# Kernel optimization log

Hardware: AMD Instinct MI355X
Metric: run time of the kernel (lower is better)

## Reference

```python
import jax, jax.numpy as jnp
import numpy as np

DIM = 4096
HEAD_DIM = 512
ROPE_DIM = 64
NOPE_DIM = HEAD_DIM - ROPE_DIM  # 448
RATIO = 4
COFF = 2  # overlap since ratio == 4
EPS = 1e-6
NEG = -1e30
COMPRESS_ROPE_THETA = 40000.0


def _hadamard(n):
    H = np.array([[1.0]], dtype=np.float32)
    while H.shape[0] < n:
        H = np.block([[H, H], [H, -H]])
    return (H / np.sqrt(n)).astype(np.float32)

H_MAT = jnp.asarray(_hadamard(HEAD_DIM))  # [512, 512], orthonormal Hadamard


def setup_inputs() -> dict:
    key = jax.random.key(0)
    ks = jax.random.split(key, 5)
    b, s = 4, 4096
    x = jax.random.normal(ks[0], (b, s, DIM), dtype=jnp.float32)
    W_kv = jax.random.normal(ks[1], (COFF * HEAD_DIM, DIM), dtype=jnp.float32) * 0.02
    W_gate = jax.random.normal(ks[2], (COFF * HEAD_DIM, DIM), dtype=jnp.float32) * 0.02
    ape = jax.random.normal(ks[3], (RATIO, COFF * HEAD_DIM), dtype=jnp.float32) * 0.02
    norm_w = jnp.ones((HEAD_DIM,), dtype=jnp.float32)
    # rotary table over compressed-block positions
    nb = s // RATIO
    inv_freq = 1.0 / (COMPRESS_ROPE_THETA ** (jnp.arange(0, ROPE_DIM, 2, dtype=jnp.float32) / ROPE_DIM))
    ang = jnp.arange(nb, dtype=jnp.float32)[:, None] * inv_freq[None, :]  # [nb, 32]
    freqs_cis = jnp.stack([jnp.cos(ang), jnp.sin(ang)], axis=-1)  # [nb, 32, 2]
    return {"x": x, "W_kv": W_kv, "W_gate": W_gate, "ape": ape,
            "norm_w": norm_w, "freqs_cis": freqs_cis, "start_pos": 0}


def _overlap_transform(t, fill):
    # t: [b, nb, RATIO, 2*d] -> [b, nb, 2*RATIO, d]
    b, nb, r, dd = t.shape
    d = dd // 2
    prev_first = jnp.concatenate(
        [jnp.full((b, 1, r, d), fill, t.dtype), t[:, :-1, :, :d]], axis=1)
    return jnp.concatenate([prev_first, t[..., d:]], axis=2)


def reference(x, W_kv, W_gate, ape, norm_w, freqs_cis, start_pos):
    b, s, _ = x.shape
    nb = s // RATIO
    # block-wise projections with absolute-within-block positional bias
    kv = jnp.einsum('bsd,od->bso', x, W_kv).reshape(b, nb, RATIO, COFF * HEAD_DIM) + ape
    score = jnp.einsum('bsd,od->bso', x, W_gate).reshape(b, nb, RATIO, COFF * HEAD_DIM)
    # overlap with previous block: [b, nb, 2*RATIO, HEAD_DIM]
    kv_w = _overlap_transform(kv, 0.0)
    sc_w = _overlap_transform(score, NEG)
    # channelwise softmax-gated pooling over the 2*RATIO window
    w = jax.nn.softmax(sc_w, axis=2)
    pooled = jnp.sum(w * kv_w, axis=2)  # [b, nb, HEAD_DIM]
    # RMSNorm
    var = jnp.mean(jnp.square(pooled), axis=-1, keepdims=True)
    pooled = norm_w * (pooled * jax.lax.rsqrt(var + EPS))
    # rotary on the rope slice
    nope, rope = pooled[..., :NOPE_DIM], pooled[..., NOPE_DIM:]
    rp = rope.reshape(b, nb, ROPE_DIM // 2, 2)
    xr, xi = rp[..., 0], rp[..., 1]
    fr, fi = freqs_cis[None, :, :, 0], freqs_cis[None, :, :, 1]
    rot = jnp.stack([xr * fr - xi * fi, xr * fi + xi * fr], axis=-1).reshape(b, nb, ROPE_DIM)
    out = jnp.concatenate([nope, rot], axis=-1)  # [b, nb, HEAD_DIM]
    # Hadamard rotation (rotate_activation)
    out = out @ H_MAT
    return out
```

## Files before the change

### kernel.cpp

```cpp
#include <hip/hip_runtime.h>
#include <hip/hip_bf16.h>
#include <stdint.h>

#define M_ROWS 16384
#define N_COLS 2048
#define K_DIM  4096
#define NEGV   -1e30f

typedef __bf16 bfv8 __attribute__((ext_vector_type(8)));
typedef float  f32x4 __attribute__((ext_vector_type(4)));
typedef unsigned short u16;

static __device__ __forceinline__ u16 f32_to_bf16_rne(float f) {
  union { float f; unsigned int u; } v; v.f = f;
  unsigned int u = v.u;
  u += 0x7fffu + ((u >> 16) & 1u);
  return (u16)(u >> 16);
}

static __device__ __forceinline__ float b2f(u16 b) {
  union { unsigned int u; float f; } v; v.u = ((unsigned int)b) << 16;
  return v.f;
}

__global__ __launch_bounds__(256) void k_cvt_x(const float* __restrict__ in,
                                               u16* __restrict__ out, long n) {
  long i = (long)blockIdx.x * blockDim.x + threadIdx.x;
  long base = i * 8;
  if (base >= n) return;
  float4 a = *(const float4*)(in + base);
  float4 b = *(const float4*)(in + base + 4);
  union { u16 s[8]; uint4 v; } o;
  o.s[0] = f32_to_bf16_rne(a.x); o.s[1] = f32_to_bf16_rne(a.y);
  o.s[2] = f32_to_bf16_rne(a.z); o.s[3] = f32_to_bf16_rne(a.w);
  o.s[4] = f32_to_bf16_rne(b.x); o.s[5] = f32_to_bf16_rne(b.y);
  o.s[6] = f32_to_bf16_rne(b.z); o.s[7] = f32_to_bf16_rne(b.w);
  *(uint4*)(out + base) = o.v;
}

__global__ __launch_bounds__(256) void k_cvt_w(const float* __restrict__ wkv,
                                               const float* __restrict__ wg,
                                               u16* __restrict__ out) {
  long i = (long)blockIdx.x * blockDim.x + threadIdx.x;
  long base = i * 8;
  const float* src = (base < 4194304L) ? (wkv + base) : (wg + (base - 4194304L));
  float4 a = *(const float4*)(src);
  float4 b = *(const float4*)(src + 4);
  union { u16 s[8]; uint4 v; } o;
  o.s[0] = f32_to_bf16_rne(a.x); o.s[1] = f32_to_bf16_rne(a.y);
  o.s[2] = f32_to_bf16_rne(a.z); o.s[3] = f32_to_bf16_rne(a.w);
  o.s[4] = f32_to_bf16_rne(b.x); o.s[5] = f32_to_bf16_rne(b.y);
  o.s[6] = f32_to_bf16_rne(b.z); o.s[7] = f32_to_bf16_rne(b.w);
  *(uint4*)(out + base) = o.v;
}

#define GLD16(g, l) __builtin_amdgcn_global_load_lds( \
    (const __attribute__((address_space(1))) unsigned int*)(g), \
    (__attribute__((address_space(3))) unsigned int*)(l), 16, 0, 0)

#define SB0 __builtin_amdgcn_sched_barrier(0)
#define BAR __builtin_amdgcn_s_barrier()
#define VM4 asm volatile("s_waitcnt vmcnt(4)" ::: "memory")

__global__ __launch_bounds__(512, 2) void k_gemm(const u16* __restrict__ A,
                                                 const u16* __restrict__ B,
                                                 u16* __restrict__ C) {
  __shared__ u16 lds[65536];

  const int tid  = threadIdx.x;
  const int wid  = tid >> 6;
  const int lane = tid & 63;
  const int wr = wid >> 2, wc = wid & 3;
  const int fr = lane & 15, fq = lane >> 4;

  int o = blockIdx.x;
  int swz = (o & 7) * 64 + (o >> 3);
  const int bm = swz >> 3, bn = swz & 7;
  const int gm0 = bm << 8, gn0 = bn << 8;

  int aoff[8], boff[4];
#pragma unroll
  for (int mi = 0; mi < 8; ++mi) {
    int row = (wr << 7) + (mi << 4) + fr;
    int Gp = (((row & 1) << 2) | fq) ^ ((row >> 1) & 7);
    aoff[mi] = (row >> 1) * 64 + Gp * 8;
  }
#pragma unroll
  for (int ni = 0; ni < 4; ++ni) {
    int row = (wc << 6) + (ni << 4) + fr;
    int Gp = (((row & 1) << 2) | fq) ^ ((row >> 1) & 7);
    boff[ni] = (row >> 1) * 64 + Gp * 8;
  }

  const int s0 = tid, s1 = 512 + tid;
  const int l0 = s0 >> 3, G0 = (s0 & 7) ^ (l0 & 7);
  const int r0 = 2 * l0 + (G0 >> 2), g0 = (G0 & 3) << 3;
  const int l1 = s1 >> 3, G1 = (s1 & 7) ^ (l1 & 7);
  const int r1 = 2 * l1 + (G1 >> 2), g1 = (G1 & 3) << 3;
  const u16* pA0 = A + ((size_t)(gm0 + r0) << 12) + g0;
  const u16* pA1 = A + ((size_t)(gm0 + r1) << 12) + g1;
  const u16* pB0 = B + ((size_t)(gn0 + r0) << 12) + g0;
  const u16* pB1 = B + ((size_t)(gn0 + r1) << 12) + g1;
  const int du0 = wid << 9;
  const int du1 = 4096 + (wid << 9);

#define STAGE_A(Q, KK, KTN) do { \
  GLD16(pA0 + (KTN) + (KK) * 32, &lds[(Q) * 16384 + (KK) * 8192 + du0]); \
  GLD16(pA1 + (KTN) + (KK) * 32, &lds[(Q) * 16384 + (KK) * 8192 + du1]); } while (0)
#define STAGE_B(Q, KK, KTN) do { \
  GLD16(pB0 + (KTN) + (KK) * 32, &lds[32768 + (Q) * 16384 + (KK) * 8192 + du0]); \
  GLD16(pB1 + (KTN) + (KK) * 32, &lds[32768 + (Q) * 16384 + (KK) * 8192 + du1]); } while (0)
#define LDA(P, KK, MI) (*(const bfv8*)&lds[(P) * 16384 + (KK) * 8192 + aoff[MI]])
#define LDB(P, KK, NI) (*(const bfv8*)&lds[32768 + (P) * 16384 + (KK) * 8192 + boff[NI]])
#define MF(AV, BV, MI, NI) acc[MI][NI] = __builtin_amdgcn_mfma_f32_16x16x32_bf16(AV, BV, acc[MI][NI], 0, 0, 0)
#define MF4(AV, MI) do { MF(AV, b0, MI, 0); MF(AV, b1, MI, 1); MF(AV, b2, MI, 2); MF(AV, b3, MI, 3); } while (0)

  f32x4 acc[8][4];
#pragma unroll
  for (int i = 0; i < 8; ++i)
#pragma unroll
    for (int j = 0; j < 4; ++j) acc[i][j] = (f32x4){0.f, 0.f, 0.f, 0.f};

  STAGE_A(0, 0, 0); STAGE_B(0, 0, 0); STAGE_A(0, 1, 0); STAGE_B(0, 1, 0);
  SB0; VM4; BAR; SB0;

  bfv8 a0, a1, a2, a3, a4, a5, a6, a7, b0, b1, b2, b3;

#define KTILE(P, Q, KTN) do { \
  a0 = LDA(P, 0, 0); a1 = LDA(P, 0, 1); a2 = LDA(P, 0, 2); a3 = LDA(P, 0, 3); \
  b0 = LDB(P, 0, 0); b1 = LDB(P, 0, 1); b2 = LDB(P, 0, 2); b3 = LDB(P, 0, 3); \
  STAGE_A(Q, 0, KTN); \
  SB0; BAR; SB0; \
  __builtin_amdgcn_s_setprio(1); \
  MF4(a0, 0); MF4(a1, 1); MF4(a2, 2); MF4(a3, 3); \
  __builtin_amdgcn_s_setprio(0); SB0; \
  a4 = LDA(P, 0, 4); a5 = LDA(P, 0, 5); a6 = LDA(P, 0, 6); a7 = LDA(P, 0, 7); \
  STAGE_B(Q, 0, KTN); \
  SB0; VM4; BAR; SB0; \
  __builtin_amdgcn_s_setprio(1); \
  MF4(a4, 4); MF4(a5, 5); MF4(a6, 6); MF4(a7, 7); \
  __builtin_amdgcn_s_setprio(0); SB0; \
  a0 = LDA(P, 1, 0); a1 = LDA(P, 1, 1); a2 = LDA(P, 1, 2); a3 = LDA(P, 1, 3); \
  b0 = LDB(P, 1, 0); b1 = LDB(P, 1, 1); b2 = LDB(P, 1, 2); b3 = LDB(P, 1, 3); \
  STAGE_A(Q, 1, KTN); \
  SB0; BAR; SB0; \
  __builtin_amdgcn_s_setprio(1); \
  MF4(a0, 0); MF4(a1, 1); MF4(a2, 2); MF4(a3, 3); \
  __builtin_amdgcn_s_setprio(0); SB0; \
  a4 = LDA(P, 1, 4); a5 = LDA(P, 1, 5); a6 = LDA(P, 1, 6); a7 = LDA(P, 1, 7); \
  STAGE_B(Q, 1, KTN); \
  SB0; VM4; BAR; SB0; \
  __builtin_amdgcn_s_setprio(1); \
  MF4(a4, 4); MF4(a5, 5); MF4(a6, 6); MF4(a7, 7); \
  __builtin_amdgcn_s_setprio(0); SB0; \
} while (0)

  for (int i = 0; i < 32; ++i) {
    const int kt1 = (2 * i + 1) << 6;
    const int kt2 = (i == 31) ? 0 : (2 * i + 2) << 6;
    KTILE(0, 1, kt1);
    KTILE(1, 0, kt2);
  }

#pragma unroll
  for (int mi = 0; mi < 8; ++mi) {
    int row = gm0 + (wr << 7) + (mi << 4) + (fq << 2);
#pragma unroll
    for (int ni = 0; ni < 4; ++ni) {
      int col = gn0 + (wc << 6) + (ni << 4) + fr;
#pragma unroll
      for (int j = 0; j < 4; ++j)
        C[(size_t)(row + j) * N_COLS + col] = f32_to_bf16_rne(acc[mi][ni][j]);
    }
  }
#undef KTILE
#undef STAGE_A
#undef STAGE_B
#undef LDA
#undef LDB
#undef MF
#undef MF4
}

__global__ __launch_bounds__(256) void k_pool(const u16* __restrict__ kvsc,
                                              const float* __restrict__ ape,
                                              const float* __restrict__ norm_w,
                                              const float* __restrict__ freqs,
                                              float* __restrict__ out) {
  __shared__ float sm[512];
  __shared__ float red[8];
  const int tid = threadIdx.x;
  const int bid = blockIdx.x;
  const int b = bid >> 10, ib = bid & 1023;

  float ss = 0.f;
#pragma unroll
  for (int cc = 0; cc < 2; ++cc) {
    int c = tid + (cc << 8);
    float kvv[8], scv[8];
    if (ib > 0) {
      size_t mb = ((size_t)b * 4096 + (size_t)(ib - 1) * 4);
#pragma unroll
      for (int p = 0; p < 4; ++p) {
        size_t ro = (mb + p) * N_COLS;
        kvv[p] = b2f(kvsc[ro + c]) + ape[p * 1024 + c];
        scv[p] = b2f(kvsc[ro + 1024 + c]);
      }
    } else {
#pragma unroll
      for (int p = 0; p < 4; ++p) { kvv[p] = 0.f; scv[p] = NEGV; }
    }
    size_t mb2 = ((size_t)b * 4096 + (size_t)ib * 4);
#pragma unroll
    for (int r = 0; r < 4; ++r) {
      size_t ro = (mb2 + r) * N_COLS;
      kvv[4 + r] = b2f(kvsc[ro + 512 + c]) + ape[r * 1024 + 512 + c];
      scv[4 + r] = b2f(kvsc[ro + 1024 + 512 + c]);
    }
    float mx = scv[0];
#pragma unroll
    for (int p = 1; p < 8; ++p) mx = fmaxf(mx, scv[p]);
    float se = 0.f, ac = 0.f;
#pragma unroll
    for (int p = 0; p < 8; ++p) {
      float e = __expf(scv[p] - mx);
      se += e; ac += e * kvv[p];
    }
    float pooled = ac / se;
    sm[c] = pooled;
    ss += pooled * pooled;
  }
#pragma unroll
  for (int m = 1; m < 64; m <<= 1) ss += __shfl_xor(ss, m, 64);
  if ((tid & 63) == 0) red[tid >> 6] = ss;
  __syncthreads();
  float sumsq = red[0] + red[1] + red[2] + red[3];
  float scale = rsqrtf(sumsq * (1.f / 512.f) + 1e-6f);
  sm[tid]       = sm[tid]       * scale * norm_w[tid];
  sm[tid + 256] = sm[tid + 256] * scale * norm_w[tid + 256];
  __syncthreads();
  if (tid < 32) {
    int j = tid;
    float xr = sm[448 + 2 * j], xi = sm[449 + 2 * j];
    float fr = freqs[((size_t)ib * 32 + j) * 2];
    float fi = freqs[((size_t)ib * 32 + j) * 2 + 1];
    sm[448 + 2 * j] = xr * fr - xi * fi;
    sm[449 + 2 * j] = xr * fi + xi * fr;
  }
  __syncthreads();
#pragma unroll
  for (int k = 0; k < 9; ++k) {
    int low = tid & ((1 << k) - 1);
    int i0 = ((tid >> k) << (k + 1)) | low;
    int i1 = i0 | (1 << k);
    float a = sm[i0], bb = sm[i1];
    sm[i0] = a + bb; sm[i1] = a - bb;
    __syncthreads();
  }
  const float OSC = 0.044194173824159216f;
  size_t ob = (size_t)bid * 512;
  out[ob + tid]       = sm[tid] * OSC;
  out[ob + tid + 256] = sm[tid + 256] * OSC;
}

extern "C" void kernel_launch(void* const* d_in, const int* in_sizes, int n_in,
                              void* d_out, int out_size, void* d_ws, size_t ws_size,
                              hipStream_t stream) {
  const float* x      = (const float*)d_in[0];
  const float* W_kv   = (const float*)d_in[1];
  const float* W_gate = (const float*)d_in[2];
  const float* ape    = (const float*)d_in[3];
  const float* norm_w = (const float*)d_in[4];
  const float* freqs  = (const float*)d_in[5];
  float* out = (float*)d_out;

  char* ws = (char*)d_ws;
  u16* xb   = (u16*)ws;
  u16* wb   = (u16*)(ws + 134217728L);
  u16* kvsc = (u16*)(ws + 134217728L + 16777216L);

  hipLaunchKernelGGL(k_cvt_x, dim3(32768), dim3(256), 0, stream, x, xb, (long)67108864L);
  hipLaunchKernelGGL(k_cvt_w, dim3(4096), dim3(256), 0, stream, W_kv, W_gate, wb);
  hipLaunchKernelGGL(k_gemm, dim3(512), dim3(512), 0, stream, xb, wb, kvsc);
  hipLaunchKernelGGL(k_pool, dim3(4096), dim3(256), 0, stream, kvsc, ape, norm_w, freqs, out);
}
```

Before: 313.7 us.

## Restructure GEMM to 4 waves with 128x128 warp tiles and interleaved pipeline

Shrinks the GEMM block from 8 waves to 4, so each wave computes a 128x128 tile with 64 accumulators instead of 8x4. The k-loop becomes fine-grained units that interleave LDS fragment loads for the next sub-step, global-to-LDS staging and MFMAs. Fragments are double-buffered in registers and the pipeline prefetches one k-step deeper. This aims to cut barriers per MFMA and raise LDS reuse, at the cost of very high register pressure and fewer waves per CU to hide latency.

After: 323.4 us. +3.1%, slower.

```diff
diff --git a/kernel.cpp b/kernel.cpp
--- a/kernel.cpp
+++ b/kernel.cpp
@@ -60,9 +60,9 @@
 
 #define SB0 __builtin_amdgcn_sched_barrier(0)
 #define BAR __builtin_amdgcn_s_barrier()
-#define VM4 asm volatile("s_waitcnt vmcnt(4)" ::: "memory")
-
-__global__ __launch_bounds__(512, 2) void k_gemm(const u16* __restrict__ A,
+#define VM8 asm volatile("s_waitcnt vmcnt(8)" ::: "memory")
+
+__global__ __launch_bounds__(256, 1) void k_gemm(const u16* __restrict__ A,
                                                  const u16* __restrict__ B,
                                                  u16* __restrict__ C) {
   __shared__ u16 lds[65536];
@@ -70,7 +70,7 @@
   const int tid  = threadIdx.x;
   const int wid  = tid >> 6;
   const int lane = tid & 63;
-  const int wr = wid >> 2, wc = wid & 3;
+  const int wr = wid >> 1, wc = wid & 1;
   const int fr = lane & 15, fq = lane >> 4;
 
   int o = blockIdx.x;
@@ -78,7 +78,7 @@
   const int bm = swz >> 3, bn = swz & 7;
   const int gm0 = bm << 8, gn0 = bn << 8;
 
-  int aoff[8], boff[4];
+  int aoff[8], boff[8];
 #pragma unroll
   for (int mi = 0; mi < 8; ++mi) {
     int row = (wr << 7) + (mi << 4) + fr;
@@ -86,100 +86,114 @@
     aoff[mi] = (row >> 1) * 64 + Gp * 8;
   }
 #pragma unroll
-  for (int ni = 0; ni < 4; ++ni) {
-    int row = (wc << 6) + (ni << 4) + fr;
+  for (int ni = 0; ni < 8; ++ni) {
+    int row = (wc << 7) + (ni << 4) + fr;
     int Gp = (((row & 1) << 2) | fq) ^ ((row >> 1) & 7);
     boff[ni] = (row >> 1) * 64 + Gp * 8;
   }
 
-  const int s0 = tid, s1 = 512 + tid;
-  const int l0 = s0 >> 3, G0 = (s0 & 7) ^ (l0 & 7);
-  const int r0 = 2 * l0 + (G0 >> 2), g0 = (G0 & 3) << 3;
-  const int l1 = s1 >> 3, G1 = (s1 & 7) ^ (l1 & 7);
-  const int r1 = 2 * l1 + (G1 >> 2), g1 = (G1 & 3) << 3;
-  const u16* pA0 = A + ((size_t)(gm0 + r0) << 12) + g0;
-  const u16* pA1 = A + ((size_t)(gm0 + r1) << 12) + g1;
-  const u16* pB0 = B + ((size_t)(gn0 + r0) << 12) + g0;
-  const u16* pB1 = B + ((size_t)(gn0 + r1) << 12) + g1;
-  const int du0 = wid << 9;
-  const int du1 = 4096 + (wid << 9);
-
-#define STAGE_A(Q, KK, KTN) do { \
-  GLD16(pA0 + (KTN) + (KK) * 32, &lds[(Q) * 16384 + (KK) * 8192 + du0]); \
-  GLD16(pA1 + (KTN) + (KK) * 32, &lds[(Q) * 16384 + (KK) * 8192 + du1]); } while (0)
-#define STAGE_B(Q, KK, KTN) do { \
-  GLD16(pB0 + (KTN) + (KK) * 32, &lds[32768 + (Q) * 16384 + (KK) * 8192 + du0]); \
-  GLD16(pB1 + (KTN) + (KK) * 32, &lds[32768 + (Q) * 16384 + (KK) * 8192 + du1]); } while (0)
+  const u16* pAs[4]; const u16* pBs[4]; int stgoff[4];
+#pragma unroll
+  for (int j = 0; j < 4; ++j) {
+    int sp = j * 256 + tid;
+    int l = sp >> 3, G = (sp & 7) ^ (l & 7);
+    int r = 2 * l + (G >> 2), g = (G & 3) << 3;
+    pAs[j] = A + ((size_t)(gm0 + r) << 12) + g;
+    pBs[j] = B + ((size_t)(gn0 + r) << 12) + g;
+    stgoff[j] = j * 2048 + (wid << 9);
+  }
+
+#define STG_A(Q, KK, J, KTN) GLD16(pAs[J] + (KTN) + (KK) * 32, &lds[(Q) * 16384 + (KK) * 8192 + stgoff[J]])
+#define STG_B(Q, KK, J, KTN) GLD16(pBs[J] + (KTN) + (KK) * 32, &lds[32768 + (Q) * 16384 + (KK) * 8192 + stgoff[J]])
 #define LDA(P, KK, MI) (*(const bfv8*)&lds[(P) * 16384 + (KK) * 8192 + aoff[MI]])
 #define LDB(P, KK, NI) (*(const bfv8*)&lds[32768 + (P) * 16384 + (KK) * 8192 + boff[NI]])
-#define MF(AV, BV, MI, NI) acc[MI][NI] = __builtin_amdgcn_mfma_f32_16x16x32_bf16(AV, BV, acc[MI][NI], 0, 0, 0)
-#define MF4(AV, MI) do { MF(AV, b0, MI, 0); MF(AV, b1, MI, 1); MF(AV, b2, MI, 2); MF(AV, b3, MI, 3); } while (0)
-
-  f32x4 acc[8][4];
+#define MFM(MI, NI, Si) acc[MI][NI] = __builtin_amdgcn_mfma_f32_16x16x32_bf16(fa[Si][MI], fb[Si][NI], acc[MI][NI], 0, 0, 0)
+
+#define UNIT(g, Pn, KKn, NSi, Si, STQ, STKK, KTN) do { \
+  if ((g) < 8) { fa[NSi][(g)] = LDA(Pn, KKn, (g)); } \
+  else         { fb[NSi][(g) - 8] = LDB(Pn, KKn, (g) - 8); } \
+  if (((g) & 1) == 0) { \
+    if ((g) < 8) { STG_A(STQ, STKK, (g) >> 1, KTN); } \
+    else         { STG_B(STQ, STKK, ((g) - 8) >> 1, KTN); } } \
+  MFM((g) >> 1, (((g) & 1) << 2) + 0, Si); \
+  MFM((g) >> 1, (((g) & 1) << 2) + 1, Si); \
+  MFM((g) >> 1, (((g) & 1) << 2) + 2, Si); \
+  MFM((g) >> 1, (((g) & 1) << 2) + 3, Si); \
+  SB0; \
+} while (0)
+
+#define PHASE(Pn, KKn, NSi, Si, STQ, STKK, KTN) do { \
+  UNIT( 0, Pn, KKn, NSi, Si, STQ, STKK, KTN); \
+  UNIT( 1, Pn, KKn, NSi, Si, STQ, STKK, KTN); \
+  UNIT( 2, Pn, KKn, NSi, Si, STQ, STKK, KTN); \
+  UNIT( 3, Pn, KKn, NSi, Si, STQ, STKK, KTN); \
+  UNIT( 4, Pn, KKn, NSi, Si, STQ, STKK, KTN); \
+  UNIT( 5, Pn, KKn, NSi, Si, STQ, STKK, KTN); \
+  UNIT( 6, Pn, KKn, NSi, Si, STQ, STKK, KTN); \
+  UNIT( 7, Pn, KKn, NSi, Si, STQ, STKK, KTN); \
+  UNIT( 8, Pn, KKn, NSi, Si, STQ, STKK, KTN); \
+  UNIT( 9, Pn, KKn, NSi, Si, STQ, STKK, KTN); \
+  UNIT(10, Pn, KKn, NSi, Si, STQ, STKK, KTN); \
+  UNIT(11, Pn, KKn, NSi, Si, STQ, STKK, KTN); \
+  UNIT(12, Pn, KKn, NSi, Si, STQ, STKK, KTN); \
+  UNIT(13, Pn, KKn, NSi, Si, STQ, STKK, KTN); \
+  UNIT(14, Pn, KKn, NSi, Si, STQ, STKK, KTN); \
+  UNIT(15, Pn, KKn, NSi, Si, STQ, STKK, KTN); \
+  VM8; BAR; SB0; \
+} while (0)
+
+  f32x4 acc[8][8];
 #pragma unroll
   for (int i = 0; i < 8; ++i)
 #pragma unroll
-    for (int j = 0; j < 4; ++j) acc[i][j] = (f32x4){0.f, 0.f, 0.f, 0.f};
-
-  STAGE_A(0, 0, 0); STAGE_B(0, 0, 0); STAGE_A(0, 1, 0); STAGE_B(0, 1, 0);
-  SB0; VM4; BAR; SB0;
-
-  bfv8 a0, a1, a2, a3, a4, a5, a6, a7, b0, b1, b2, b3;
-
-#define KTILE(P, Q, KTN) do { \
-  a0 = LDA(P, 0, 0); a1 = LDA(P, 0, 1); a2 = LDA(P, 0, 2); a3 = LDA(P, 0, 3); \
-  b0 = LDB(P, 0, 0); b1 = LDB(P, 0, 1); b2 = LDB(P, 0, 2); b3 = LDB(P, 0, 3); \
-  STAGE_A(Q, 0, KTN); \
-  SB0; BAR; SB0; \
-  __builtin_amdgcn_s_setprio(1); \
-  MF4(a0, 0); MF4(a1, 1); MF4(a2, 2); MF4(a3, 3); \
-  __builtin_amdgcn_s_setprio(0); SB0; \
-  a4 = LDA(P, 0, 4); a5 = LDA(P, 0, 5); a6 = LDA(P, 0, 6); a7 = LDA(P, 0, 7); \
-  STAGE_B(Q, 0, KTN); \
-  SB0; VM4; BAR; SB0; \
-  __builtin_amdgcn_s_setprio(1); \
-  MF4(a4, 4); MF4(a5, 5); MF4(a6, 6); MF4(a7, 7); \
-  __builtin_amdgcn_s_setprio(0); SB0; \
-  a0 = LDA(P, 1, 0); a1 = LDA(P, 1, 1); a2 = LDA(P, 1, 2); a3 = LDA(P, 1, 3); \
-  b0 = LDB(P, 1, 0); b1 = LDB(P, 1, 1); b2 = LDB(P, 1, 2); b3 = LDB(P, 1, 3); \
-  STAGE_A(Q, 1, KTN); \
-  SB0; BAR; SB0; \
-  __builtin_amdgcn_s_setprio(1); \
-  MF4(a0, 0); MF4(a1, 1); MF4(a2, 2); MF4(a3, 3); \
-  __builtin_amdgcn_s_setprio(0); SB0; \
-  a4 = LDA(P, 1, 4); a5 = LDA(P, 1, 5); a6 = LDA(P, 1, 6); a7 = LDA(P, 1, 7); \
-  STAGE_B(Q, 1, KTN); \
-  SB0; VM4; BAR; SB0; \
-  __builtin_amdgcn_s_setprio(1); \
-  MF4(a4, 4); MF4(a5, 5); MF4(a6, 6); MF4(a7, 7); \
-  __builtin_amdgcn_s_setprio(0); SB0; \
-} while (0)
+    for (int j = 0; j < 8; ++j) acc[i][j] = (f32x4){0.f, 0.f, 0.f, 0.f};
+
+  bfv8 fa[2][8], fb[2][8];
+
+#pragma unroll
+  for (int j = 0; j < 4; ++j) STG_A(0, 0, j, 0);
+#pragma unroll
+  for (int j = 0; j < 4; ++j) STG_B(0, 0, j, 0);
+#pragma unroll
+  for (int j = 0; j < 4; ++j) STG_A(0, 1, j, 0);
+#pragma unroll
+  for (int j = 0; j < 4; ++j) STG_B(0, 1, j, 0);
+#pragma unroll
+  for (int j = 0; j < 4; ++j) STG_A(1, 0, j, 64);
+#pragma unroll
+  for (int j = 0; j < 4; ++j) STG_B(1, 0, j, 64);
+  SB0; VM8; BAR; SB0;
+#pragma unroll
+  for (int g = 0; g < 8; ++g) { fa[0][g] = LDA(0, 0, g); fb[0][g] = LDB(0, 0, g); }
 
   for (int i = 0; i < 32; ++i) {
-    const int kt1 = (2 * i + 1) << 6;
-    const int kt2 = (i == 31) ? 0 : (2 * i + 2) << 6;
-    KTILE(0, 1, kt1);
-    KTILE(1, 0, kt2);
+    const int ktB = ((2 * i + 1) & 63) << 6;
+    const int ktC = ((2 * i + 2) & 63) << 6;
+    const int ktD = ((2 * i + 3) & 63) << 6;
+    PHASE(0, 1, 1, 0, 1, 1, ktB);
+    PHASE(1, 0, 0, 1, 0, 0, ktC);
+    PHASE(1, 1, 1, 0, 0, 1, ktC);
+    PHASE(0, 0, 0, 1, 1, 0, ktD);
   }
 
 #pragma unroll
   for (int mi = 0; mi < 8; ++mi) {
     int row = gm0 + (wr << 7) + (mi << 4) + (fq << 2);
 #pragma unroll
-    for (int ni = 0; ni < 4; ++ni) {
-      int col = gn0 + (wc << 6) + (ni << 4) + fr;
+    for (int ni = 0; ni < 8; ++ni) {
+      int col = gn0 + (wc << 7) + (ni << 4) + fr;
 #pragma unroll
       for (int j = 0; j < 4; ++j)
         C[(size_t)(row + j) * N_COLS + col] = f32_to_bf16_rne(acc[mi][ni][j]);
     }
   }
-#undef KTILE
-#undef STAGE_A
-#undef STAGE_B
+#undef PHASE
+#undef UNIT
+#undef STG_A
+#undef STG_B
 #undef LDA
 #undef LDB
-#undef MF
-#undef MF4
+#undef MFM
 }
 
 __global__ __launch_bounds__(256) void k_pool(const u16* __restrict__ kvsc,
@@ -281,6 +295,6 @@
 
   hipLaunchKernelGGL(k_cvt_x, dim3(32768), dim3(256), 0, stream, x, xb, (long)67108864L);
   hipLaunchKernelGGL(k_cvt_w, dim3(4096), dim3(256), 0, stream, W_kv, W_gate, wb);
-  hipLaunchKernelGGL(k_gemm, dim3(512), dim3(512), 0, stream, xb, wb, kvsc);
+  hipLaunchKernelGGL(k_gemm, dim3(512), dim3(256), 0, stream, xb, wb, kvsc);
   hipLaunchKernelGGL(k_pool, dim3(4096), dim3(256), 0, stream, kvsc, ape, norm_w, freqs, out);
 }
```
